# Optimization experiments

Hardware: AMD Instinct MI355X
Metric: run time of the kernel (lower is better)

## Reference

```python
import jax, jax.numpy as jnp
import numpy as np

B, L, E, C = 256, 1024, 128, 5  # trees, leaves per tree, embed size, num classes

def setup_inputs() -> dict:
    key = jax.random.key(0)
    k1, k2, k3 = jax.random.split(key, 3)
    leaves = jax.random.normal(k1, (B, L, E), dtype=jnp.float32)
    # Glorot-ish scaling so 10 stacked relu(Linear) levels stay well-conditioned
    W = jax.random.normal(k2, (E, 2 * E), dtype=jnp.float32) * (2.0 / (2 * E)) ** 0.5
    bW = jnp.zeros((E,), dtype=jnp.float32)
    P = jax.random.normal(k3, (C, E), dtype=jnp.float32) * (2.0 / E) ** 0.5
    bP = jnp.zeros((C,), dtype=jnp.float32)
    return {"leaves": leaves, "W": W, "bW": bW, "P": P, "bP": bP}

def reference(leaves, W, bW, P, bP):
    """Batched level-by-level bottom-up pass over a forest of perfect binary trees.
    Per internal node (same math as RecursiveNN.traverse):
        h = relu(W @ concat(left, right) + bW)
        proj = P @ h + bP
    Returns all internal-node projections concatenated: [B*(L-1), C].
    """
    x = leaves  # [B, n, E] current frontier of node embeddings
    probs = []
    while x.shape[1] > 1:
        # pair adjacent siblings: [B, n/2, 2E]
        pairs = jnp.concatenate([x[:, 0::2], x[:, 1::2]], axis=-1)
        h = jax.nn.relu(jnp.einsum('bnf,ef->bne', pairs, W) + bW)  # [B, n/2, E]
        proj = jnp.einsum('bne,ce->bnc', h, P) + bP                # [B, n/2, C]
        probs.append(proj.reshape(-1, P.shape[0]))
        x = h
    return jnp.concatenate(probs, axis=0)  # [B*(L-1), C]
```

## Files before the change

### kernel.cpp

```cpp
#include <hip/hip_runtime.h>
#include <hip/hip_bf16.h>
#include <hip/hip_fp16.h>


typedef _Float16 f16_t;
typedef _Float16 f16x4 __attribute__((ext_vector_type(4)));
typedef _Float16 f16x8 __attribute__((ext_vector_type(8)));
typedef float f32x4 __attribute__((ext_vector_type(4)));

#define HSTRIDE 136

static __device__ __forceinline__ f32x4 mfma16(f16x8 a, f16x8 b, f32x4 c) {
    return __builtin_amdgcn_mfma_f32_16x16x32_f16(a, b, c, 0, 0, 0);
}

static __device__ __forceinline__ f16x8 cvt8(const float* p) {
    const float4 a = *(const float4*)p;
    const float4 b = *(const float4*)(p + 4);
    f16x8 t = { (f16_t)a.x, (f16_t)a.y, (f16_t)a.z, (f16_t)a.w,
                (f16_t)b.x, (f16_t)b.y, (f16_t)b.z, (f16_t)b.w };
    return t;
}

__global__ __launch_bounds__(256, 3)
void forest_kernel(const float* __restrict__ leaves,
                   const float* __restrict__ W,
                   const float* __restrict__ P,
                   const float* __restrict__ bW,
                   const float* __restrict__ bP,
                   f16_t* __restrict__ Q,
                   float* __restrict__ out)
{
    __shared__ f16_t Stg[2][32 * HSTRIDE];
    __shared__ f16_t Hbuf[128 * HSTRIDE];

    const int tid   = threadIdx.x;
    const int wave  = tid >> 6;
    const int lane  = tid & 63;
    const int mlane = lane & 15;
    const int q     = lane >> 4;
    const int tree  = blockIdx.x >> 2;
    const int qq    = blockIdx.x & 3;
    const size_t m0 = (size_t)blockIdx.x * 128;
    const float* leafbase = leaves + (size_t)blockIdx.x * 32768;

    auto store_stage = [&](int buf, const float4* pf) {
        #pragma unroll
        for (int r = 0; r < 4; ++r) {
            const int idx = tid + r * 256;
            const int row = idx >> 5;
            const int c4  = idx & 31;
            f16x4 t4 = { (f16_t)pf[r].x, (f16_t)pf[r].y, (f16_t)pf[r].z, (f16_t)pf[r].w };
            *(f16x4*)&Stg[buf][row * HSTRIDE + c4 * 4] = t4;
        }
    };

    float4 pf[4];
    #pragma unroll
    for (int r = 0; r < 4; ++r) pf[r] = ((const float4*)leafbase)[tid + r * 256];

    f16x8 wh[2][8];
    float bwv[2];
    #pragma unroll
    for (int n = 0; n < 2; ++n) {
        const int col = wave * 32 + n * 16 + mlane;
        bwv[n] = bW[col];
        #pragma unroll
        for (int k = 0; k < 8; ++k)
            wh[n][k] = cvt8(&W[col * 256 + k * 32 + q * 8]);
    }

    f16x8 pb[4] = {};
    if (mlane < 5) {
        #pragma unroll
        for (int kb = 0; kb < 4; ++kb)
            pb[kb] = cvt8(&P[mlane * 128 + kb * 32 + q * 8]);
    }
    const float bpv = (mlane < 5) ? bP[mlane] : 0.f;

    store_stage(0, pf);

    auto proj_store = [&](int hrow0, size_t orow0, int valid) {
        f32x4 pc = {};
        #pragma unroll
        for (int kb = 0; kb < 4; ++kb) {
            const f16x8 ha = *(const f16x8*)&Hbuf[(hrow0 + mlane) * HSTRIDE + kb * 32 + q * 8];
            pc = mfma16(ha, pb[kb], pc);
        }
        if (mlane < 5) {
            #pragma unroll
            for (int r = 0; r < 4; ++r) {
                const int row = q * 4 + r;
                if (row < valid) out[(orow0 + row) * 5 + mlane] = pc[r] + bpv;
            }
        }
    };

    for (int c = 0; c < 8; ++c) {
        __syncthreads();
        if (c < 7) {
            #pragma unroll
            for (int r = 0; r < 4; ++r)
                pf[r] = ((const float4*)leafbase)[(c + 1) * 1024 + tid + r * 256];
        }
        f16x8 af[8];
        const f16_t* sb = Stg[c & 1];
        #pragma unroll
        for (int k = 0; k < 8; ++k) {
            const int off  = k * 64 + q * 16;
            const int trow = off >> 8;
            const int ce   = (off & 255) >> 1;
            af[k] = *(const f16x8*)&sb[(2 * mlane + trow) * HSTRIDE + ce];
        }
        f32x4 acc0 = {}, acc1 = {};
        #pragma unroll
        for (int k = 0; k < 8; ++k) {
            acc0 = mfma16(af[k], wh[0][k], acc0);
            acc1 = mfma16(af[k], wh[1][k], acc1);
        }
        if (c < 7) store_stage((c + 1) & 1, pf);

        #pragma unroll
        for (int r = 0; r < 4; ++r) {
            float v0 = fmaxf(acc0[r] + bwv[0], 0.f);
            float v1 = fmaxf(acc1[r] + bwv[1], 0.f);
            Hbuf[(c * 16 + q * 4 + r) * HSTRIDE + wave * 32 + mlane]      = (f16_t)v0;
            Hbuf[(c * 16 + q * 4 + r) * HSTRIDE + wave * 32 + 16 + mlane] = (f16_t)v1;
        }
        __syncthreads();

        if (wave == 0) proj_store(c * 16, m0 + c * 16, 16);
    }

    int Mprev = 128;
    #pragma unroll 1
    for (int j = 2; j <= 8; ++j) {
        const int Mnew   = Mprev >> 1;
        const int chunks = (Mnew + 15) >> 4;
        const size_t off_j = 256 * (1024 - (2048 >> j));
        for (int c = 0; c < chunks; ++c) {
            f16x8 af[8];
            #pragma unroll
            for (int k = 0; k < 8; ++k) {
                const int off  = k * 64 + q * 16;
                const int trow = off >> 8;
                const int ce   = (off & 255) >> 1;
                af[k] = *(const f16x8*)&Hbuf[(32 * c + 2 * mlane + trow) * HSTRIDE + ce];
            }
            __syncthreads();
            f32x4 acc0 = {}, acc1 = {};
            #pragma unroll
            for (int k = 0; k < 8; ++k) {
                acc0 = mfma16(af[k], wh[0][k], acc0);
                acc1 = mfma16(af[k], wh[1][k], acc1);
            }
            #pragma unroll
            for (int r = 0; r < 4; ++r) {
                float v0 = fmaxf(acc0[r] + bwv[0], 0.f);
                float v1 = fmaxf(acc1[r] + bwv[1], 0.f);
                Hbuf[(c * 16 + q * 4 + r) * HSTRIDE + wave * 32 + mlane]      = (f16_t)v0;
                Hbuf[(c * 16 + q * 4 + r) * HSTRIDE + wave * 32 + 16 + mlane] = (f16_t)v1;
            }
            __syncthreads();

            const int valid = (Mnew - c * 16 < 16) ? (Mnew - c * 16) : 16;
            if (wave == 0)
                proj_store(c * 16,
                           off_j + (size_t)tree * (Mnew * 4) + (size_t)qq * Mnew + c * 16,
                           valid);
        }
        Mprev = Mnew;
    }

    if (tid < 16)
        *(uint4*)&Q[(size_t)blockIdx.x * 128 + tid * 8] = *(const uint4*)&Hbuf[tid * 8];
}

__global__ __launch_bounds__(128, 4)
void rnn_top_kernel(const f16_t* __restrict__ Q,
                    const float* __restrict__ W,
                    const float* __restrict__ bW,
                    const float* __restrict__ P,
                    const float* __restrict__ bP,
                    float* __restrict__ out)
{
    __shared__ float qs[512];
    __shared__ float hs[384];
    const int t    = threadIdx.x;
    const int tree = blockIdx.x;

    #pragma unroll
    for (int i = 0; i < 4; ++i)
        qs[t + i * 128] = (float)Q[(size_t)tree * 512 + t + i * 128];
    __syncthreads();

    const float* wr = W + t * 256;
    float s0 = bW[t], s1 = s0;
    for (int k = 0; k < 256; k += 4) {
        const float4 wv = *(const float4*)(wr + k);
        s0 += wv.x * qs[k]     + wv.y * qs[k + 1]     + wv.z * qs[k + 2]     + wv.w * qs[k + 3];
        s1 += wv.x * qs[256+k] + wv.y * qs[256+k + 1] + wv.z * qs[256+k + 2] + wv.w * qs[256+k + 3];
    }
    hs[t]       = fmaxf(s0, 0.f);
    hs[128 + t] = fmaxf(s1, 0.f);
    __syncthreads();

    float s2 = bW[t];
    for (int k = 0; k < 256; k += 4) {
        const float4 wv = *(const float4*)(wr + k);
        s2 += wv.x * hs[k] + wv.y * hs[k + 1] + wv.z * hs[k + 2] + wv.w * hs[k + 3];
    }
    hs[256 + t] = fmaxf(s2, 0.f);
    __syncthreads();

    if (t < 15) {
        const int node = t / 5, c = t % 5;
        float s = bP[c];
        for (int k = 0; k < 128; ++k) s += hs[node * 128 + k] * P[c * 128 + k];
        const size_t row = (node < 2) ? (261120 + (size_t)tree * 2 + node)
                                      : (261632 + (size_t)tree);
        out[row * 5 + c] = s;
    }
}

extern "C" void kernel_launch(void* const* d_in, const int* in_sizes, int n_in,
                              void* d_out, int out_size, void* d_ws, size_t ws_size,
                              hipStream_t stream) {
    const float* leaves = (const float*)d_in[0];
    const float* W      = (const float*)d_in[1];
    const float* bW     = (const float*)d_in[2];
    const float* P      = (const float*)d_in[3];
    const float* bP     = (const float*)d_in[4];
    float* out = (float*)d_out;

    f16_t* Q = (f16_t*)d_ws;

    forest_kernel<<<dim3(1024), dim3(256), 0, stream>>>(leaves, W, P, bW, bP, Q, out);
    rnn_top_kernel<<<dim3(256), dim3(128), 0, stream>>>(Q, W, bW, P, bP, out);
}
```

Before: 262.0 us.

## Split each tree across eight blocks and move one more level to top kernel

The forest kernel now gives each block 128 leaves instead of 256, launching 2048 blocks, and stops one level earlier. The top kernel takes over that extra level (four nodes per tree) in scalar fp32 before the last two levels. Smaller Hbuf and more blocks are meant to improve occupancy and load balance across CUs. In exchange the serial top kernel does more work, and launch bounds drop to 2 blocks per SM.

```diff
diff --git a/kernel.cpp b/kernel.cpp
--- a/kernel.cpp
+++ b/kernel.cpp
@@ -22,7 +22,7 @@
     return t;
 }
 
-__global__ __launch_bounds__(256, 3)
+__global__ __launch_bounds__(256, 2)
 void forest_kernel(const float* __restrict__ leaves,
                    const float* __restrict__ W,
                    const float* __restrict__ P,
@@ -32,17 +32,17 @@
                    float* __restrict__ out)
 {
     __shared__ f16_t Stg[2][32 * HSTRIDE];
-    __shared__ f16_t Hbuf[128 * HSTRIDE];
+    __shared__ f16_t Hbuf[64 * HSTRIDE];
 
     const int tid   = threadIdx.x;
     const int wave  = tid >> 6;
     const int lane  = tid & 63;
     const int mlane = lane & 15;
     const int q     = lane >> 4;
-    const int tree  = blockIdx.x >> 2;
-    const int qq    = blockIdx.x & 3;
-    const size_t m0 = (size_t)blockIdx.x * 128;
-    const float* leafbase = leaves + (size_t)blockIdx.x * 32768;
+    const int tree  = blockIdx.x >> 3;
+    const int e     = blockIdx.x & 7;
+    const size_t m0 = (size_t)blockIdx.x * 64;
+    const float* leafbase = leaves + (size_t)blockIdx.x * 16384;
 
     auto store_stage = [&](int buf, const float4* pf) {
         #pragma unroll
@@ -96,9 +96,9 @@
         }
     };
 
-    for (int c = 0; c < 8; ++c) {
+    for (int c = 0; c < 4; ++c) {
         __syncthreads();
-        if (c < 7) {
+        if (c < 3) {
             #pragma unroll
             for (int r = 0; r < 4; ++r)
                 pf[r] = ((const float4*)leafbase)[(c + 1) * 1024 + tid + r * 256];
@@ -118,7 +118,7 @@
             acc0 = mfma16(af[k], wh[0][k], acc0);
             acc1 = mfma16(af[k], wh[1][k], acc1);
         }
-        if (c < 7) store_stage((c + 1) & 1, pf);
+        if (c < 3) store_stage((c + 1) & 1, pf);
 
         #pragma unroll
         for (int r = 0; r < 4; ++r) {
@@ -132,12 +132,13 @@
         if (wave == 0) proj_store(c * 16, m0 + c * 16, 16);
     }
 
-    int Mprev = 128;
+    int Mprev = 64;
     #pragma unroll 1
-    for (int j = 2; j <= 8; ++j) {
+    for (int j = 2; j <= 7; ++j) {
         const int Mnew   = Mprev >> 1;
         const int chunks = (Mnew + 15) >> 4;
         const size_t off_j = 256 * (1024 - (2048 >> j));
+        const size_t base_j = off_j + (size_t)tree * (1024 >> j) + (size_t)e * (128 >> j);
         for (int c = 0; c < chunks; ++c) {
             f16x8 af[8];
             #pragma unroll
@@ -165,9 +166,7 @@
 
             const int valid = (Mnew - c * 16 < 16) ? (Mnew - c * 16) : 16;
             if (wave == 0)
-                proj_store(c * 16,
-                           off_j + (size_t)tree * (Mnew * 4) + (size_t)qq * Mnew + c * 16,
-                           valid);
+                proj_store(c * 16, base_j + c * 16, valid);
         }
         Mprev = Mnew;
     }
@@ -184,41 +183,65 @@
                     const float* __restrict__ bP,
                     float* __restrict__ out)
 {
-    __shared__ float qs[512];
-    __shared__ float hs[384];
+    __shared__ float qs[1024];
+    __shared__ float hs[896];
     const int t    = threadIdx.x;
     const int tree = blockIdx.x;
 
     #pragma unroll
-    for (int i = 0; i < 4; ++i)
-        qs[t + i * 128] = (float)Q[(size_t)tree * 512 + t + i * 128];
+    for (int i = 0; i < 8; ++i)
+        qs[t + i * 128] = (float)Q[(size_t)tree * 1024 + t + i * 128];
     __syncthreads();
 
     const float* wr = W + t * 256;
-    float s0 = bW[t], s1 = s0;
+
+    float s8[4];
+    #pragma unroll
+    for (int n = 0; n < 4; ++n) s8[n] = bW[t];
     for (int k = 0; k < 256; k += 4) {
         const float4 wv = *(const float4*)(wr + k);
-        s0 += wv.x * qs[k]     + wv.y * qs[k + 1]     + wv.z * qs[k + 2]     + wv.w * qs[k + 3];
-        s1 += wv.x * qs[256+k] + wv.y * qs[256+k + 1] + wv.z * qs[256+k + 2] + wv.w * qs[256+k + 3];
-    }
-    hs[t]       = fmaxf(s0, 0.f);
-    hs[128 + t] = fmaxf(s1, 0.f);
-    __syncthreads();
-
-    float s2 = bW[t];
+        #pragma unroll
+        for (int n = 0; n < 4; ++n) {
+            const float* qb = qs + n * 256 + k;
+            s8[n] += wv.x * qb[0] + wv.y * qb[1] + wv.z * qb[2] + wv.w * qb[3];
+        }
+    }
+    #pragma unroll
+    for (int n = 0; n < 4; ++n) hs[n * 128 + t] = fmaxf(s8[n], 0.f);
+    __syncthreads();
+
+    float s9[2];
+    s9[0] = s9[1] = bW[t];
     for (int k = 0; k < 256; k += 4) {
         const float4 wv = *(const float4*)(wr + k);
-        s2 += wv.x * hs[k] + wv.y * hs[k + 1] + wv.z * hs[k + 2] + wv.w * hs[k + 3];
-    }
-    hs[256 + t] = fmaxf(s2, 0.f);
-    __syncthreads();
-
-    if (t < 15) {
+        #pragma unroll
+        for (int m = 0; m < 2; ++m) {
+            const float* hb = hs + m * 256 + k;
+            s9[m] += wv.x * hb[0] + wv.y * hb[1] + wv.z * hb[2] + wv.w * hb[3];
+        }
+    }
+    hs[512 + t] = fmaxf(s9[0], 0.f);
+    hs[640 + t] = fmaxf(s9[1], 0.f);
+    __syncthreads();
+
+    float s10 = bW[t];
+    for (int k = 0; k < 256; k += 4) {
+        const float4 wv = *(const float4*)(wr + k);
+        const float* hb = hs + 512 + k;
+        s10 += wv.x * hb[0] + wv.y * hb[1] + wv.z * hb[2] + wv.w * hb[3];
+    }
+    hs[768 + t] = fmaxf(s10, 0.f);
+    __syncthreads();
+
+    if (t < 35) {
         const int node = t / 5, c = t % 5;
         float s = bP[c];
-        for (int k = 0; k < 128; ++k) s += hs[node * 128 + k] * P[c * 128 + k];
-        const size_t row = (node < 2) ? (261120 + (size_t)tree * 2 + node)
-                                      : (261632 + (size_t)tree);
+        const float* hb = hs + node * 128;
+        for (int k = 0; k < 128; ++k) s += hb[k] * P[c * 128 + k];
+        size_t row;
+        if (node < 4)      row = 260096 + (size_t)tree * 4 + node;
+        else if (node < 6) row = 261120 + (size_t)tree * 2 + (node - 4);
+        else               row = 261632 + (size_t)tree;
         out[row * 5 + c] = s;
     }
 }
@@ -235,6 +258,6 @@
 
     f16_t* Q = (f16_t*)d_ws;
 
-    forest_kernel<<<dim3(1024), dim3(256), 0, stream>>>(leaves, W, P, bW, bP, Q, out);
+    forest_kernel<<<dim3(2048), dim3(256), 0, stream>>>(leaves, W, P, bW, bP, Q, out);
     rnn_top_kernel<<<dim3(256), dim3(128), 0, stream>>>(Q, W, bW, P, bP, out);
 }
```

Measured after the change: 248.0 us. 5.3% less time.
